# Performance work log

Hardware: AMD Instinct MI355X
Metric: run time of the kernel (lower is better)

## Reference

```python
import jax, jax.numpy as jnp
import numpy as np

IN_F = 2048
OUT_F = 2048
BATCH = 8192
ACT_BITS = 4
EPS = 1e-5


def setup_inputs() -> dict:
    key = jax.random.key(0)
    kx, kw, kb = jax.random.split(key, 3)
    x = jax.random.normal(kx, (BATCH, IN_F), dtype=jnp.float32)
    # kaiming-uniform-like init: bound = sqrt(6/fan_in) with a=sqrt(5) -> gain sqrt(2/(1+5))
    bound_w = float(np.sqrt(6.0 / (1.0 + 5.0)) / np.sqrt(IN_F))
    weight = jax.random.uniform(kw, (OUT_F, IN_F), minval=-bound_w, maxval=bound_w, dtype=jnp.float32)
    bound_b = float(1.0 / np.sqrt(IN_F))
    bias = jax.random.uniform(kb, (OUT_F,), minval=-bound_b, maxval=bound_b, dtype=jnp.float32)
    return {"x": x, "weight": weight, "bias": bias}


def _ste_sign(x):
    return x + jax.lax.stop_gradient(jnp.sign(x) - x)


def _ste_clip(x, lo, hi):
    return x + jax.lax.stop_gradient(jnp.clip(x, lo, hi) - x)


def reference(x, weight, bias):
    # weight binarization (ternary-ish via sign of mean-centered rows)
    w_centered = weight - jnp.mean(weight, axis=1, keepdims=True)
    w_bin = _ste_sign(w_centered)                       # [out, in]
    beta = jnp.mean(jnp.abs(weight), axis=1)[None, :]   # [1, out]
    # layer norm (no affine) over last dim
    mu = jnp.mean(x, axis=-1, keepdims=True)
    var = jnp.mean((x - mu) ** 2, axis=-1, keepdims=True)
    xln = (x - mu) / jnp.sqrt(var + EPS)
    qb = float(2 ** (ACT_BITS - 1) - 1)
    gama = jnp.maximum(jnp.max(jnp.abs(xln), axis=-1, keepdims=True), EPS)  # [B,1]
    xq = _ste_clip(xln * (qb / gama), -qb + EPS, qb - EPS)
    y = jnp.einsum('bi,oi->bo', xq, w_bin)
    y = y * (beta * gama / qb)
    return y + bias
```

## Files before the change

### kernel.cpp

```cpp
#include <hip/hip_runtime.h>
#include <hip/hip_bf16.h>

#define BATCH 8192
#define IN_F  2048
#define OUT_F 2048
#define QB    7.0f
#define EPSV  1e-5f
#define ASCALE 18.0f

typedef char  i8x4 __attribute__((ext_vector_type(4)));
typedef int   i32x4 __attribute__((ext_vector_type(4)));

#define AS1(p) ((__attribute__((address_space(1))) void*)(p))
#define AS3(p) ((__attribute__((address_space(3))) void*)(p))

__global__ __launch_bounds__(256) void prep_kernel(const float* __restrict__ x,
                                                   const float* __restrict__ w,
                                                   char* __restrict__ xq,
                                                   char* __restrict__ wb,
                                                   float* __restrict__ gamaOut,
                                                   float* __restrict__ betaOut) {
  const int t = threadIdx.x;
  const int wave = t >> 6, lane = t & 63;
  const int rowId = blockIdx.x * 4 + wave;

  if (rowId < OUT_F) {
    const int row = rowId;
    const float4* wr = (const float4*)(w + (size_t)row * IN_F);
    float4 v[8];
#pragma unroll
    for (int j = 0; j < 8; ++j) v[j] = wr[lane + 64 * j];

    float s = 0.0f, sa = 0.0f;
#pragma unroll
    for (int j = 0; j < 8; ++j) {
      s  += v[j].x + v[j].y + v[j].z + v[j].w;
      sa += fabsf(v[j].x) + fabsf(v[j].y) + fabsf(v[j].z) + fabsf(v[j].w);
    }
#pragma unroll
    for (int off = 32; off > 0; off >>= 1) {
      s  += __shfl_xor(s, off, 64);
      sa += __shfl_xor(sa, off, 64);
    }
    const float mu = s * (1.0f / IN_F);
    if (lane == 0) betaOut[row] = sa * (1.0f / IN_F);

    char* wbr = wb + (size_t)row * IN_F;
    auto sgn = [&](float xv) -> char {
      float d = xv - mu;
      return (char)((d > 0.0f) ? 1 : (d < 0.0f ? -1 : 0));
    };
#pragma unroll
    for (int j = 0; j < 8; ++j) {
      i8x4 q = { sgn(v[j].x), sgn(v[j].y), sgn(v[j].z), sgn(v[j].w) };
      ((i8x4*)wbr)[lane + 64 * j] = q;
    }
  } else {
    const int row = rowId - OUT_F;
    const float4* xr = (const float4*)(x + (size_t)row * IN_F);
    float4 v[8];
#pragma unroll
    for (int j = 0; j < 8; ++j) v[j] = xr[lane + 64 * j];

    float s = 0.0f, s2 = 0.0f;
#pragma unroll
    for (int j = 0; j < 8; ++j) {
      s  += v[j].x + v[j].y + v[j].z + v[j].w;
      s2 += v[j].x * v[j].x + v[j].y * v[j].y + v[j].z * v[j].z + v[j].w * v[j].w;
    }
#pragma unroll
    for (int off = 32; off > 0; off >>= 1) {
      s  += __shfl_xor(s, off, 64);
      s2 += __shfl_xor(s2, off, 64);
    }
    const float mu   = s * (1.0f / IN_F);
    const float rstd = rsqrtf(fmaxf(s2 * (1.0f / IN_F) - mu * mu, 0.0f) + EPSV);

    float ad = 0.0f;
#pragma unroll
    for (int j = 0; j < 8; ++j) {
      ad = fmaxf(ad, fmaxf(fmaxf(fabsf(v[j].x - mu), fabsf(v[j].y - mu)),
                           fmaxf(fabsf(v[j].z - mu), fabsf(v[j].w - mu))));
    }
#pragma unroll
    for (int off = 32; off > 0; off >>= 1) ad = fmaxf(ad, __shfl_xor(ad, off, 64));
    const float g = fmaxf(ad * rstd, EPSV);
    if (lane == 0) gamaOut[row] = g;

    const float c  = rstd * (QB * ASCALE) / g;
    const float lo = (-QB + EPSV) * ASCALE, hi = (QB - EPSV) * ASCALE;
    auto qz = [&](float vv) -> char {
      return (char)__float2int_rn(fminf(fmaxf((vv - mu) * c, lo), hi));
    };
    char* xqr = xq + (size_t)row * IN_F;
#pragma unroll
    for (int j = 0; j < 8; ++j) {
      i8x4 q = { qz(v[j].x), qz(v[j].y), qz(v[j].z), qz(v[j].w) };
      ((i8x4*)xqr)[lane + 64 * j] = q;
    }
  }
}

__global__ __launch_bounds__(512) void gemm_kernel(const char* __restrict__ A,
                                                   const char* __restrict__ B,
                                                   const float* __restrict__ beta,
                                                   const float* __restrict__ gama,
                                                   const float* __restrict__ bias,
                                                   float* __restrict__ out) {
  __shared__ __align__(16) char As[2 * 256 * 128];
  __shared__ __align__(16) char Bs[2 * 256 * 128];

  const int t = threadIdx.x;
  const int wave = t >> 6, lane = t & 63;
  const int bid = blockIdx.x;
  const int swz = (bid & 7) * 32 + (bid >> 3);
  const int mBase = (swz >> 3) * 256;
  const int nBase = (swz & 7) * 256;
  const int wm = (wave >> 2) * 128;
  const int wn = (wave & 3) * 64;

  i32x4 acc[8][4];
#pragma unroll
  for (int i = 0; i < 8; ++i)
#pragma unroll
    for (int j = 0; j < 4; ++j) {
      i32x4 z = {0, 0, 0, 0};
      acc[i][j] = z;
    }

  const int lr = lane >> 3;
  const int ls = lane & 7;
  const int gch = (ls - lr) & 7;
  const char* aG[4];
  const char* bG[4];
  int lOff[4];
#pragma unroll
  for (int j = 0; j < 4; ++j) {
    const int rowInTile = j * 64 + wave * 8 + lr;
    aG[j] = A + (size_t)(mBase + rowInTile) * IN_F + gch * 16;
    bG[j] = B + (size_t)(nBase + rowInTile) * IN_F + gch * 16;
    lOff[j] = (j * 64 + wave * 8) * 128;
  }

  const int fr = lane & 15;
  const int kq = lane >> 4;
  int koff[2];
#pragma unroll
  for (int ks = 0; ks < 2; ++ks) koff[ks] = ((ks * 4 + kq + fr) & 7) * 16;

  auto stage = [&](int k0, int buf) {
#pragma unroll
    for (int j = 0; j < 4; ++j) {
      __builtin_amdgcn_global_load_lds(AS1(aG[j] + k0), AS3(As + buf * 32768 + lOff[j]), 16, 0, 0);
      __builtin_amdgcn_global_load_lds(AS1(bG[j] + k0), AS3(Bs + buf * 32768 + lOff[j]), 16, 0, 0);
    }
  };
  auto compute = [&](int buf) {
    const char* aF = As + buf * 32768 + (wm + fr) * 128;
    const char* bF = Bs + buf * 32768 + (wn + fr) * 128;
#pragma unroll
    for (int ks = 0; ks < 2; ++ks) {
      i32x4 af[8], bf[4];
#pragma unroll
      for (int mi = 0; mi < 8; ++mi) af[mi] = *(const i32x4*)(aF + mi * 16 * 128 + koff[ks]);
#pragma unroll
      for (int ni = 0; ni < 4; ++ni) bf[ni] = *(const i32x4*)(bF + ni * 16 * 128 + koff[ks]);
#pragma unroll
      for (int mi = 0; mi < 8; ++mi)
#pragma unroll
        for (int ni = 0; ni < 4; ++ni)
          acc[mi][ni] = __builtin_amdgcn_mfma_i32_16x16x64_i8(af[mi], bf[ni], acc[mi][ni], 0, 0, 0);
    }
  };

  stage(0, 0);
  __syncthreads();

  int cur = 0;
  for (int k0 = 128; k0 < IN_F; k0 += 128) {
    stage(k0, cur ^ 1);
    compute(cur);
    __syncthreads();
    cur ^= 1;
  }
  compute(cur);

  const float qinv = 1.0f / (QB * ASCALE);
  const int orow0 = mBase + wm + (kq << 2);
  const int ocol0 = nBase + wn + fr;
#pragma unroll
  for (int mi = 0; mi < 8; ++mi) {
    const int rbase = orow0 + mi * 16;
    const float g0 = gama[rbase + 0] * qinv;
    const float g1 = gama[rbase + 1] * qinv;
    const float g2 = gama[rbase + 2] * qinv;
    const float g3 = gama[rbase + 3] * qinv;
#pragma unroll
    for (int ni = 0; ni < 4; ++ni) {
      const int c = ocol0 + ni * 16;
      const float bsc = beta[c];
      const float bv  = bias[c];
      float* op = out + (size_t)rbase * OUT_F + c;
      op[0 * OUT_F] = (float)acc[mi][ni][0] * (bsc * g0) + bv;
      op[1 * OUT_F] = (float)acc[mi][ni][1] * (bsc * g1) + bv;
      op[2 * OUT_F] = (float)acc[mi][ni][2] * (bsc * g2) + bv;
      op[3 * OUT_F] = (float)acc[mi][ni][3] * (bsc * g3) + bv;
    }
  }
}

extern "C" void kernel_launch(void* const* d_in, const int* in_sizes, int n_in,
                              void* d_out, int out_size, void* d_ws, size_t ws_size,
                              hipStream_t stream) {
  const float* x      = (const float*)d_in[0];
  const float* weight = (const float*)d_in[1];
  const float* bias   = (const float*)d_in[2];
  float* out = (float*)d_out;

  char* ws = (char*)d_ws;
  char* wbin = ws;
  char* xq   = ws + (size_t)OUT_F * IN_F;
  float* betaW = (float*)(ws + (size_t)OUT_F * IN_F + (size_t)BATCH * IN_F);
  float* gamaX = betaW + OUT_F;

  prep_kernel<<<(OUT_F + BATCH) / 4, 256, 0, stream>>>(x, weight, xq, wbin, gamaX, betaW);
  gemm_kernel<<<(OUT_F / 256) * (BATCH / 256), 512, 0, stream>>>(xq, wbin, betaW, gamaX, bias, out);
}
```

Before: 160.7 us.

## Restructure int8 GEMM main loop into fine-grained interleaved load/MFMA phases

The GEMM K-tile is split into two 64-byte halves with a new LDS layout and swizzle. Each iteration becomes four phases that interleave global-to-LDS prefetch of the next tile, LDS fragment reads and 16-MFMA bursts, using explicit vmcnt/lgkmcnt waits, raw barriers and setprio around the MFMAs. The aim is to overlap memory traffic with matrix work and reduce register pressure by holding only half of the A fragments at once. The cost is many more barriers per iteration and fragile hand-managed wait counts.

```diff
diff --git a/kernel.cpp b/kernel.cpp
--- a/kernel.cpp
+++ b/kernel.cpp
@@ -13,6 +13,11 @@
 
 #define AS1(p) ((__attribute__((address_space(1))) void*)(p))
 #define AS3(p) ((__attribute__((address_space(3))) void*)(p))
+
+#define SBAR()  __builtin_amdgcn_s_barrier()
+#define LGKM0() do { asm volatile("s_waitcnt lgkmcnt(0)" ::: "memory"); \
+                     __builtin_amdgcn_sched_barrier(0); } while (0)
+#define WAIT_VM(N) asm volatile("s_waitcnt vmcnt(" #N ")" ::: "memory")
 
 __global__ __launch_bounds__(256) void prep_kernel(const float* __restrict__ x,
                                                    const float* __restrict__ w,
@@ -101,14 +106,14 @@
   }
 }
 
-__global__ __launch_bounds__(512) void gemm_kernel(const char* __restrict__ A,
-                                                   const char* __restrict__ B,
-                                                   const float* __restrict__ beta,
-                                                   const float* __restrict__ gama,
-                                                   const float* __restrict__ bias,
-                                                   float* __restrict__ out) {
-  __shared__ __align__(16) char As[2 * 256 * 128];
-  __shared__ __align__(16) char Bs[2 * 256 * 128];
+__global__ __launch_bounds__(512, 1) void gemm_kernel(const char* __restrict__ A,
+                                                      const char* __restrict__ B,
+                                                      const float* __restrict__ beta,
+                                                      const float* __restrict__ gama,
+                                                      const float* __restrict__ bias,
+                                                      float* __restrict__ out) {
+  __shared__ __align__(16) char As[2 * 2 * 256 * 64];
+  __shared__ __align__(16) char Bs[2 * 2 * 256 * 64];
 
   const int t = threadIdx.x;
   const int wave = t >> 6, lane = t & 63;
@@ -128,62 +133,94 @@
       acc[i][j] = z;
     }
 
-  const int lr = lane >> 3;
-  const int ls = lane & 7;
-  const int gch = (ls - lr) & 7;
-  const char* aG[4];
-  const char* bG[4];
-  int lOff[4];
-#pragma unroll
-  for (int j = 0; j < 4; ++j) {
-    const int rowInTile = j * 64 + wave * 8 + lr;
-    aG[j] = A + (size_t)(mBase + rowInTile) * IN_F + gch * 16;
-    bG[j] = B + (size_t)(nBase + rowInTile) * IN_F + gch * 16;
-    lOff[j] = (j * 64 + wave * 8) * 128;
-  }
+  const int lr2 = lane >> 2;
+  const int ls2 = lane & 3;
+  const int krot = (ls2 - (lr2 >> 1)) & 3;
+  const char* aGg = A + (size_t)(mBase + wave * 16 + lr2) * IN_F + krot * 16;
+  const char* bGg = B + (size_t)(nBase + wave * 16 + lr2) * IN_F + krot * 16;
+
+  auto stageA = [&](int k0, int buf, int h, int j) {
+    __builtin_amdgcn_global_load_lds(
+        AS1(aGg + (size_t)j * 128 * IN_F + k0 + h * 64),
+        AS3(As + buf * 32768 + h * 16384 + (j * 128 + wave * 16) * 64), 16, 0, 0);
+  };
+  auto stageB = [&](int k0, int buf, int h, int j) {
+    __builtin_amdgcn_global_load_lds(
+        AS1(bGg + (size_t)j * 128 * IN_F + k0 + h * 64),
+        AS3(Bs + buf * 32768 + h * 16384 + (j * 128 + wave * 16) * 64), 16, 0, 0);
+  };
 
   const int fr = lane & 15;
   const int kq = lane >> 4;
-  int koff[2];
-#pragma unroll
-  for (int ks = 0; ks < 2; ++ks) koff[ks] = ((ks * 4 + kq + fr) & 7) * 16;
-
-  auto stage = [&](int k0, int buf) {
-#pragma unroll
-    for (int j = 0; j < 4; ++j) {
-      __builtin_amdgcn_global_load_lds(AS1(aG[j] + k0), AS3(As + buf * 32768 + lOff[j]), 16, 0, 0);
-      __builtin_amdgcn_global_load_lds(AS1(bG[j] + k0), AS3(Bs + buf * 32768 + lOff[j]), 16, 0, 0);
-    }
-  };
-  auto compute = [&](int buf) {
-    const char* aF = As + buf * 32768 + (wm + fr) * 128;
-    const char* bF = Bs + buf * 32768 + (wn + fr) * 128;
-#pragma unroll
-    for (int ks = 0; ks < 2; ++ks) {
-      i32x4 af[8], bf[4];
-#pragma unroll
-      for (int mi = 0; mi < 8; ++mi) af[mi] = *(const i32x4*)(aF + mi * 16 * 128 + koff[ks]);
-#pragma unroll
-      for (int ni = 0; ni < 4; ++ni) bf[ni] = *(const i32x4*)(bF + ni * 16 * 128 + koff[ks]);
-#pragma unroll
-      for (int mi = 0; mi < 8; ++mi)
-#pragma unroll
-        for (int ni = 0; ni < 4; ++ni)
-          acc[mi][ni] = __builtin_amdgcn_mfma_i32_16x16x64_i8(af[mi], bf[ni], acc[mi][ni], 0, 0, 0);
-    }
-  };
-
-  stage(0, 0);
-  __syncthreads();
-
-  int cur = 0;
-  for (int k0 = 128; k0 < IN_F; k0 += 128) {
-    stage(k0, cur ^ 1);
-    compute(cur);
-    __syncthreads();
-    cur ^= 1;
+  const int slot = (kq + (fr >> 1)) & 3;
+  const int aRd = (wm + fr) * 64 + slot * 16;
+  const int bRd = (wn + fr) * 64 + slot * 16;
+
+  auto ldA = [&](i32x4* af, int buf, int ks, int miBase) {
+#pragma unroll
+    for (int mi = 0; mi < 4; ++mi)
+      af[mi] = *(const i32x4*)(As + buf * 32768 + ks * 16384 + aRd + (miBase + mi) * 1024);
+  };
+  auto ldB = [&](i32x4* bf, int buf, int ks) {
+#pragma unroll
+    for (int ni = 0; ni < 4; ++ni)
+      bf[ni] = *(const i32x4*)(Bs + buf * 32768 + ks * 16384 + bRd + ni * 1024);
+  };
+  auto mfma16 = [&](const i32x4* af, const i32x4* bf, int miBase) {
+    __builtin_amdgcn_s_setprio(1);
+#pragma unroll
+    for (int mi = 0; mi < 4; ++mi)
+#pragma unroll
+      for (int ni = 0; ni < 4; ++ni)
+        acc[miBase + mi][ni] =
+            __builtin_amdgcn_mfma_i32_16x16x64_i8(af[mi], bf[ni], acc[miBase + mi][ni], 0, 0, 0);
+    __builtin_amdgcn_s_setprio(0);
+  };
+
+  stageA(0, 0, 0, 0); stageA(0, 0, 0, 1);
+  stageB(0, 0, 0, 0); stageB(0, 0, 0, 1);
+  stageA(0, 0, 1, 0); stageA(0, 0, 1, 1);
+  stageB(0, 0, 1, 0); stageB(0, 0, 1, 1);
+  WAIT_VM(4);
+  SBAR();
+
+  int buf = 0;
+  for (int k0 = 0; k0 < IN_F; k0 += 128) {
+    const bool pf = (k0 + 128 < IN_F);
+    const int nk = k0 + 128;
+    const int nb = buf ^ 1;
+    i32x4 af[4], bf[4];
+
+    ldB(bf, buf, 0);
+    ldA(af, buf, 0, 0);
+    if (pf) { stageA(nk, nb, 0, 0); stageA(nk, nb, 0, 1); }
+    SBAR(); LGKM0();
+    mfma16(af, bf, 0);
+    SBAR();
+
+    ldA(af, buf, 0, 4);
+    if (pf) { stageB(nk, nb, 0, 0); stageB(nk, nb, 0, 1); }
+    if (pf) { WAIT_VM(4); } else { WAIT_VM(0); }
+    SBAR(); LGKM0();
+    mfma16(af, bf, 4);
+    SBAR();
+
+    ldB(bf, buf, 1);
+    ldA(af, buf, 1, 0);
+    if (pf) { stageA(nk, nb, 1, 0); stageA(nk, nb, 1, 1); }
+    SBAR(); LGKM0();
+    mfma16(af, bf, 0);
+    SBAR();
+
+    ldA(af, buf, 1, 4);
+    if (pf) { stageB(nk, nb, 1, 0); stageB(nk, nb, 1, 1); }
+    if (pf) { WAIT_VM(4); }
+    SBAR(); LGKM0();
+    mfma16(af, bf, 4);
+    SBAR();
+
+    buf = nb;
   }
-  compute(cur);
 
   const float qinv = 1.0f / (QB * ASCALE);
   const int orow0 = mBase + wm + (kq << 2);
```

New measurement: 159.9 us. No clear change (-0.5%).
